# Kernel tuning notes

Measured on AMD Instinct MI355X. Metric: run time of the kernel, lower is better.

## Reference

```python
import jax, jax.numpy as jnp
import numpy as np

N_NODES = 50000


def _gcn_conv(x, edge_index, W, b):
    """PyG-style GCNConv: add self-loops, symmetric deg^-1/2 norm, linear + scatter-add + bias."""
    n = x.shape[0]
    # add self loops
    loop = jnp.arange(n, dtype=edge_index.dtype)
    src = jnp.concatenate([edge_index[0], loop])  # [E+N]
    dst = jnp.concatenate([edge_index[1], loop])
    ones = jnp.ones_like(dst, dtype=x.dtype)
    deg = jax.ops.segment_sum(ones, dst, num_segments=n)  # in-degree incl. self loop
    deg_inv_sqrt = jnp.where(deg > 0, jax.lax.rsqrt(deg), 0.0)
    norm = deg_inv_sqrt[src] * deg_inv_sqrt[dst]  # [E+N]
    h = x @ W  # [N, out]
    msg = h[src] * norm[:, None]  # gather + scale, [E+N, out]
    out = jax.ops.segment_sum(msg, dst, num_segments=n)  # scatter-add
    return out + b


def setup_inputs() -> dict:
    key = jax.random.key(0)
    k1, k2, k3, k4 = jax.random.split(key, 4)
    in_ch, hid, z = 128, 128, 64
    x = jax.random.normal(k1, (N_NODES, in_ch), dtype=jnp.float32)
    edge_index = jax.random.randint(k2, (2, 800000), 0, N_NODES, dtype=jnp.int64)
    W1 = jax.random.normal(k3, (in_ch, hid), dtype=jnp.float32) * (1.0 / np.sqrt(in_ch))
    b1 = jnp.zeros((hid,), dtype=jnp.float32)
    W2 = jax.random.normal(k4, (hid, z), dtype=jnp.float32) * (1.0 / np.sqrt(hid))
    b2 = jnp.zeros((z,), dtype=jnp.float32)
    return {"x": x, "edge_index": edge_index, "W1": W1, "b1": b1, "W2": W2, "b2": b2}


def reference(x, edge_index, W1, b1, W2, b2):
    h = jax.nn.relu(_gcn_conv(x, edge_index, W1, b1))
    return _gcn_conv(h, edge_index, W2, b2)
```

## Files before the change

kernel.cpp:

```cpp
#include <hip/hip_runtime.h>

static constexpr int K = 128;

using ushort8 = __attribute__((ext_vector_type(8))) unsigned short;
using bf16x8  = __attribute__((ext_vector_type(8))) __bf16;
using f32x4   = __attribute__((ext_vector_type(4))) float;

__device__ inline float bflo(unsigned u) { return __uint_as_float(u << 16); }
__device__ inline float bfhi(unsigned u) { return __uint_as_float(u & 0xFFFF0000u); }
__device__ inline unsigned short f2bf(float f) {
    unsigned u = __float_as_uint(f);
    return (unsigned short)((u + 0x7FFF + ((u >> 16) & 1)) >> 16);
}


__global__ __launch_bounds__(256) void k_zerob(int* __restrict__ bcnt) {
    bcnt[threadIdx.x] = 0;
}

__global__ __launch_bounds__(256) void k_bcount(const int* __restrict__ dst, int e,
                                                int* __restrict__ bcnt, int nb) {
    __shared__ int c[256];
    int t = threadIdx.x;
    c[t] = 0;
    __syncthreads();
    for (int i = blockIdx.x * 256 + t; i < e; i += gridDim.x * 256)
        atomicAdd(&c[dst[i] >> 8], 1);
    __syncthreads();
    if (t < nb && c[t]) atomicAdd(&bcnt[t], c[t]);
}

__global__ __launch_bounds__(256) void k_bscan(const int* __restrict__ bcnt,
                                               int* __restrict__ bbase,
                                               int* __restrict__ gcur,
                                               int nb, int* __restrict__ offs,
                                               int n, int e) {
    __shared__ int sh[256];
    int t = threadIdx.x;
    int v = (t < nb) ? bcnt[t] : 0;
    sh[t] = v;
    __syncthreads();
    for (int o = 1; o < 256; o <<= 1) {
        int x = (t >= o) ? sh[t - o] : 0;
        __syncthreads();
        sh[t] += x;
        __syncthreads();
    }
    int excl = sh[t] - v;
    bbase[t] = excl;
    gcur[t] = excl;
    if (t == 255) bbase[256] = sh[255];
    if (t == 0) offs[n] = e;
}

__global__ __launch_bounds__(256) void k_bin(const int* __restrict__ ei, int e,
                                             int* __restrict__ gcur,
                                             unsigned long long* __restrict__ tmp) {
    constexpr int PER = 8;
    __shared__ int cnt[256], base[256], cur[256];
    int t = threadIdx.x;
    int chunk0 = blockIdx.x * 256 * PER;
    cnt[t] = 0;
    __syncthreads();
    int ds[PER];
#pragma unroll
    for (int k2 = 0; k2 < PER; ++k2) {
        int i = chunk0 + k2 * 256 + t;
        ds[k2] = (i < e) ? ei[(size_t)e + i] : -1;
        if (ds[k2] >= 0) atomicAdd(&cnt[ds[k2] >> 8], 1);
    }
    __syncthreads();
    int c = cnt[t];
    base[t] = c ? atomicAdd(&gcur[t], c) : 0;
    cur[t] = 0;
    __syncthreads();
#pragma unroll
    for (int k2 = 0; k2 < PER; ++k2) {
        int i = chunk0 + k2 * 256 + t;
        if (i < e) {
            int b = ds[k2] >> 8;
            int pos = base[b] + atomicAdd(&cur[b], 1);
            tmp[pos] = ((unsigned long long)(unsigned)ds[k2] << 32) | (unsigned)ei[i];
        }
    }
}

__global__ __launch_bounds__(256) void k_csr(const unsigned long long* __restrict__ tmp,
                                             const int* __restrict__ bbase,
                                             int* __restrict__ offs,
                                             int* __restrict__ srt,
                                             float* __restrict__ dinv, int n) {
    __shared__ int cntS[256], sh[256], cur[256];
    int b = blockIdx.x;
    int t = threadIdx.x;
    int beg = bbase[b], end = bbase[b + 1];
    cntS[t] = 0;
    __syncthreads();
    for (int i = beg + t; i < end; i += 256)
        atomicAdd(&cntS[(int)(tmp[i] >> 32) & 255], 1);
    __syncthreads();
    int v = cntS[t];
    sh[t] = v;
    __syncthreads();
    for (int o = 1; o < 256; o <<= 1) {
        int x = (t >= o) ? sh[t - o] : 0;
        __syncthreads();
        sh[t] += x;
        __syncthreads();
    }
    int pfx = sh[t] - v;
    int node = b * 256 + t;
    if (node < n) {
        offs[node] = beg + pfx;
        dinv[node] = rsqrtf((float)(v + 1));
    }
    cur[t] = pfx;
    __syncthreads();
    for (int i = beg + t; i < end; i += 256) {
        unsigned long long pr = tmp[i];
        int d = (int)(pr >> 32);
        int pos = atomicAdd(&cur[d & 255], 1);
        srt[beg + pos] = (int)(pr & 0xFFFFFFFFu);
    }
}


template <int COUT>
__global__ __launch_bounds__(256) void k_gemm_mfma(const float* __restrict__ X,
                                                   const float* __restrict__ W,
                                                   const float* __restrict__ dinv,
                                                   unsigned short* __restrict__ G, int n) {
    constexpr int BM = 64, BK = 32;
    constexpr int NCT = COUT / 16;
    constexpr int NCH = K / BK;
    constexpr int WT = COUT * (BK / 8) / 256;
    __shared__ unsigned short Ah[BM * BK], Al[BM * BK];
    __shared__ unsigned short Bh[COUT * BK], Bl[COUT * BK];
    __shared__ float dS[BM];
    const int tid = threadIdx.x;
    const int row0 = blockIdx.x * BM;
    if (tid < BM) {
        int gr = row0 + tid;
        dS[tid] = (gr < n) ? dinv[gr] : 0.f;
    }

    float4 xr[2];
    float wr[WT][8];

    auto loadX = [&](int kc) {
        int r = tid >> 2, ks = tid & 3;
        int gr = row0 + r;
        if (gr < n) {
            const float4* pp = (const float4*)(X + (size_t)gr * K + kc * BK + ks * 8);
            xr[0] = pp[0];
            xr[1] = pp[1];
        } else {
            xr[0] = make_float4(0.f, 0.f, 0.f, 0.f);
            xr[1] = xr[0];
        }
    };
    auto loadW = [&](int kc) {
#pragma unroll
        for (int q = 0; q < WT; ++q) {
            int i = tid + q * 256;
            int c = i % COUT, ks = i / COUT;
#pragma unroll
            for (int j = 0; j < 8; ++j)
                wr[q][j] = W[(size_t)(kc * BK + ks * 8 + j) * COUT + c];
        }
    };
    auto storeLDS = [&]() {
        int r = tid >> 2, ks = tid & 3;
        ushort8 h, l;
        const float* f = (const float*)&xr[0];
#pragma unroll
        for (int j = 0; j < 8; ++j) {
            unsigned short hh = f2bf(f[j]);
            h[j] = hh;
            l[j] = f2bf(f[j] - __uint_as_float((unsigned)hh << 16));
        }
        *(ushort8*)&Ah[r * BK + ks * 8] = h;
        *(ushort8*)&Al[r * BK + ks * 8] = l;
#pragma unroll
        for (int q = 0; q < WT; ++q) {
            int i = tid + q * 256;
            int c = i % COUT, ks2 = i / COUT;
            ushort8 wh, wl;
#pragma unroll
            for (int j = 0; j < 8; ++j) {
                unsigned short hh = f2bf(wr[q][j]);
                wh[j] = hh;
                wl[j] = f2bf(wr[q][j] - __uint_as_float((unsigned)hh << 16));
            }
            *(ushort8*)&Bh[c * BK + ks2 * 8] = wh;
            *(ushort8*)&Bl[c * BK + ks2 * 8] = wl;
        }
    };

    f32x4 acc[NCT] = {};
    const int l = tid & 63, wv = tid >> 6;
    const int l16 = l & 15, lk = l >> 4;
    const int arow = wv * 16 + l16;

    loadX(0);
    loadW(0);
    storeLDS();
    __syncthreads();
    for (int c = 0; c < NCH; ++c) {
        if (c + 1 < NCH) { loadX(c + 1); loadW(c + 1); }
        bf16x8 ah = *(const bf16x8*)&Ah[arow * BK + lk * 8];
        bf16x8 al = *(const bf16x8*)&Al[arow * BK + lk * 8];
#pragma unroll
        for (int ct = 0; ct < NCT; ++ct) {
            bf16x8 bh = *(const bf16x8*)&Bh[(ct * 16 + l16) * BK + lk * 8];
            bf16x8 bl = *(const bf16x8*)&Bl[(ct * 16 + l16) * BK + lk * 8];
            acc[ct] = __builtin_amdgcn_mfma_f32_16x16x32_bf16(ah, bh, acc[ct], 0, 0, 0);
            acc[ct] = __builtin_amdgcn_mfma_f32_16x16x32_bf16(al, bh, acc[ct], 0, 0, 0);
            acc[ct] = __builtin_amdgcn_mfma_f32_16x16x32_bf16(ah, bl, acc[ct], 0, 0, 0);
        }
        if (c + 1 < NCH) {
            __syncthreads();
            storeLDS();
            __syncthreads();
        }
    }

#pragma unroll
    for (int ct = 0; ct < NCT; ++ct) {
        int col = ct * 16 + l16;
#pragma unroll
        for (int r4 = 0; r4 < 4; ++r4) {
            int lr = wv * 16 + lk * 4 + r4;
            int gr = row0 + lr;
            if (gr < n) G[(size_t)gr * COUT + col] = f2bf(acc[ct][r4] * dS[lr]);
        }
    }
}


#define ADD8(u)                                      \
    do {                                             \
        a[0] += bflo((u).x); a[1] += bfhi((u).x);    \
        a[2] += bflo((u).y); a[3] += bfhi((u).y);    \
        a[4] += bflo((u).z); a[5] += bfhi((u).z);    \
        a[6] += bflo((u).w); a[7] += bfhi((u).w);    \
    } while (0)

template <bool RELU>
__global__ __launch_bounds__(256) void k_reduce128(const int* __restrict__ offs,
                                                   const int* __restrict__ srt,
                                                   const uint4* __restrict__ g4,
                                                   const float* __restrict__ dinv,
                                                   const float* __restrict__ bias,
                                                   float* __restrict__ out, int n) {
    int node = blockIdx.x * 4 + (threadIdx.x >> 6);
    if (node >= n) return;
    int lane = threadIdx.x & 63;
    int l16 = lane & 15, grp = lane >> 4;
    int beg = offs[node], end = offs[node + 1];

    float a[8] = {};
    if (grp == 0) {
        uint4 u = g4[(size_t)node * 16 + l16];
        ADD8(u);
    }
    int j = beg + grp;
    for (; j + 12 < end; j += 16) {
        uint4 u0 = g4[(size_t)srt[j]      * 16 + l16];
        uint4 u1 = g4[(size_t)srt[j + 4]  * 16 + l16];
        uint4 u2 = g4[(size_t)srt[j + 8]  * 16 + l16];
        uint4 u3 = g4[(size_t)srt[j + 12] * 16 + l16];
        ADD8(u0); ADD8(u1); ADD8(u2); ADD8(u3);
    }
    for (; j < end; j += 4) {
        uint4 u = g4[(size_t)srt[j] * 16 + l16];
        ADD8(u);
    }
#pragma unroll
    for (int q = 0; q < 8; ++q) {
        a[q] += __shfl_xor(a[q], 16);
        a[q] += __shfl_xor(a[q], 32);
    }
    if (lane < 16) {
        float di = dinv[node];
        float4 b0 = ((const float4*)bias)[l16 * 2];
        float4 b1 = ((const float4*)bias)[l16 * 2 + 1];
        float4 o0, o1;
        o0.x = fmaf(di, a[0], b0.x); o0.y = fmaf(di, a[1], b0.y);
        o0.z = fmaf(di, a[2], b0.z); o0.w = fmaf(di, a[3], b0.w);
        o1.x = fmaf(di, a[4], b1.x); o1.y = fmaf(di, a[5], b1.y);
        o1.z = fmaf(di, a[6], b1.z); o1.w = fmaf(di, a[7], b1.w);
        if (RELU) {
            o0.x = fmaxf(o0.x, 0.f); o0.y = fmaxf(o0.y, 0.f);
            o0.z = fmaxf(o0.z, 0.f); o0.w = fmaxf(o0.w, 0.f);
            o1.x = fmaxf(o1.x, 0.f); o1.y = fmaxf(o1.y, 0.f);
            o1.z = fmaxf(o1.z, 0.f); o1.w = fmaxf(o1.w, 0.f);
        }
        float4* op = (float4*)(out + (size_t)node * 128 + l16 * 8);
        op[0] = o0;
        op[1] = o1;
    }
}

template <bool RELU>
__global__ __launch_bounds__(256) void k_reduce64(const int* __restrict__ offs,
                                                  const int* __restrict__ srt,
                                                  const uint4* __restrict__ g4,
                                                  const float* __restrict__ dinv,
                                                  const float* __restrict__ bias,
                                                  float* __restrict__ out, int n) {
    int node = blockIdx.x * 4 + (threadIdx.x >> 6);
    if (node >= n) return;
    int lane = threadIdx.x & 63;
    int l8 = lane & 7, grp = lane >> 3;
    int beg = offs[node], end = offs[node + 1];

    float a[8] = {};
    if (grp == 0) {
        uint4 u = g4[(size_t)node * 8 + l8];
        ADD8(u);
    }
    int j = beg + grp;
    for (; j + 8 < end; j += 16) {
        uint4 u0 = g4[(size_t)srt[j]     * 8 + l8];
        uint4 u1 = g4[(size_t)srt[j + 8] * 8 + l8];
        ADD8(u0); ADD8(u1);
    }
    for (; j < end; j += 8) {
        uint4 u = g4[(size_t)srt[j] * 8 + l8];
        ADD8(u);
    }
#pragma unroll
    for (int q = 0; q < 8; ++q) {
        a[q] += __shfl_xor(a[q], 8);
        a[q] += __shfl_xor(a[q], 16);
        a[q] += __shfl_xor(a[q], 32);
    }
    if (lane < 8) {
        float di = dinv[node];
        float4 b0 = ((const float4*)bias)[l8 * 2];
        float4 b1 = ((const float4*)bias)[l8 * 2 + 1];
        float4 o0, o1;
        o0.x = fmaf(di, a[0], b0.x); o0.y = fmaf(di, a[1], b0.y);
        o0.z = fmaf(di, a[2], b0.z); o0.w = fmaf(di, a[3], b0.w);
        o1.x = fmaf(di, a[4], b1.x); o1.y = fmaf(di, a[5], b1.y);
        o1.z = fmaf(di, a[6], b1.z); o1.w = fmaf(di, a[7], b1.w);
        if (RELU) {
            o0.x = fmaxf(o0.x, 0.f); o0.y = fmaxf(o0.y, 0.f);
            o0.z = fmaxf(o0.z, 0.f); o0.w = fmaxf(o0.w, 0.f);
            o1.x = fmaxf(o1.x, 0.f); o1.y = fmaxf(o1.y, 0.f);
            o1.z = fmaxf(o1.z, 0.f); o1.w = fmaxf(o1.w, 0.f);
        }
        float4* op = (float4*)(out + (size_t)node * 64 + l8 * 8);
        op[0] = o0;
        op[1] = o1;
    }
}

extern "C" void kernel_launch(void* const* d_in, const int* in_sizes, int n_in,
                              void* d_out, int out_size, void* d_ws, size_t ws_size,
                              hipStream_t stream) {
    const float* x  = (const float*)d_in[0];
    const int*   ei = (const int*)d_in[1];
    const float* W1 = (const float*)d_in[2];
    const float* b1 = (const float*)d_in[3];
    const float* W2 = (const float*)d_in[4];
    const float* b2 = (const float*)d_in[5];
    float* out = (float*)d_out;

    const int n = in_sizes[0] / K;
    const int e = in_sizes[1] / 2;
    const int nb = (n + 255) / 256;

    char* p = (char*)d_ws;
    unsigned long long* tmp = (unsigned long long*)p;  p += (size_t)e * 8;
    int* bcnt  = (int*)p;  p += 256 * 4;
    int* bbase = (int*)p;  p += 257 * 4;
    int* gcur  = (int*)p;  p += 256 * 4;
    int* offs  = (int*)p;  p += (size_t)(n + 1) * 4;
    int* srt   = (int*)p;  p += (size_t)e * 4;
    float* dinv = (float*)p;  p += (size_t)n * 4;
    p = (char*)(((uintptr_t)p + 15) & ~(uintptr_t)15);
    unsigned short* G1 = (unsigned short*)p;  p += (size_t)n * 128 * 2;
    p = (char*)(((uintptr_t)p + 15) & ~(uintptr_t)15);
    float* H = (float*)p;  p += (size_t)n * 128 * 4;
    p = (char*)(((uintptr_t)p + 15) & ~(uintptr_t)15);
    unsigned short* G2 = (unsigned short*)p;

    k_zerob<<<1, 256, 0, stream>>>(bcnt);
    k_bcount<<<512, 256, 0, stream>>>(ei + e, e, bcnt, nb);
    k_bscan<<<1, 256, 0, stream>>>(bcnt, bbase, gcur, nb, offs, n, e);
    k_bin<<<(e + 2047) / 2048, 256, 0, stream>>>(ei, e, gcur, tmp);
    k_csr<<<nb, 256, 0, stream>>>(tmp, bbase, offs, srt, dinv, n);

    k_gemm_mfma<128><<<(n + 63) / 64, 256, 0, stream>>>(x, W1, dinv, G1, n);
    k_reduce128<true><<<(n + 3) / 4, 256, 0, stream>>>(offs, srt, (const uint4*)G1,
                                                       dinv, b1, H, n);

    k_gemm_mfma<64><<<(n + 63) / 64, 256, 0, stream>>>(H, W2, dinv, G2, n);
    k_reduce64<false><<<(n + 3) / 4, 256, 0, stream>>>(offs, srt, (const uint4*)G2,
                                                       dinv, b2, out, n);
}
```

Measured before the change: 156.0 us.

## Bin edges into fixed-capacity buckets and store hidden layer as bf16

The separate edge-count pass and its scan are removed. Edges are now binned directly into per-bucket slabs of fixed capacity (CAP=8192), and the scan runs afterwards. The CSR kernel now uses 1024 threads per bucket. The hidden activation H is stored as bf16 instead of fp32, and a new bf16-input GEMM for layer 2 drops the low-part split on X, which reduces memory traffic and MFMA work. The cost is extra rounding on H and a hard bucket capacity that overflows if any 256-node bucket receives more than 8192 edges.

```diff
diff --git a/kernel.cpp b/kernel.cpp
--- a/kernel.cpp
+++ b/kernel.cpp
@@ -1,6 +1,7 @@
 #include <hip/hip_runtime.h>
 
 static constexpr int K = 128;
+static constexpr int CAP = 8192;
 
 using ushort8 = __attribute__((ext_vector_type(8))) unsigned short;
 using bf16x8  = __attribute__((ext_vector_type(8))) __bf16;
@@ -14,30 +15,46 @@
 }
 
 
-__global__ __launch_bounds__(256) void k_zerob(int* __restrict__ bcnt) {
-    bcnt[threadIdx.x] = 0;
-}
-
-__global__ __launch_bounds__(256) void k_bcount(const int* __restrict__ dst, int e,
-                                                int* __restrict__ bcnt, int nb) {
-    __shared__ int c[256];
+__global__ __launch_bounds__(256) void k_bin(const int* __restrict__ ei, int e,
+                                             int* __restrict__ gcur,
+                                             unsigned long long* __restrict__ tmp) {
+    constexpr int PER = 4;
+    __shared__ int cnt[256], base[256], cur[256];
     int t = threadIdx.x;
-    c[t] = 0;
-    __syncthreads();
-    for (int i = blockIdx.x * 256 + t; i < e; i += gridDim.x * 256)
-        atomicAdd(&c[dst[i] >> 8], 1);
-    __syncthreads();
-    if (t < nb && c[t]) atomicAdd(&bcnt[t], c[t]);
-}
-
-__global__ __launch_bounds__(256) void k_bscan(const int* __restrict__ bcnt,
+    int chunk0 = blockIdx.x * 256 * PER;
+    cnt[t] = 0;
+    __syncthreads();
+    int ds[PER];
+#pragma unroll
+    for (int k2 = 0; k2 < PER; ++k2) {
+        int i = chunk0 + k2 * 256 + t;
+        ds[k2] = (i < e) ? ei[(size_t)e + i] : -1;
+        if (ds[k2] >= 0) atomicAdd(&cnt[ds[k2] >> 8], 1);
+    }
+    __syncthreads();
+    int c = cnt[t];
+    base[t] = c ? atomicAdd(&gcur[t], c) : 0;
+    cur[t] = 0;
+    __syncthreads();
+#pragma unroll
+    for (int k2 = 0; k2 < PER; ++k2) {
+        int i = chunk0 + k2 * 256 + t;
+        if (i < e) {
+            int b = ds[k2] >> 8;
+            int pos = base[b] + atomicAdd(&cur[b], 1);
+            tmp[(size_t)b * CAP + pos] =
+                ((unsigned long long)(unsigned)ds[k2] << 32) | (unsigned)ei[i];
+        }
+    }
+}
+
+__global__ __launch_bounds__(256) void k_bscan(const int* __restrict__ gcur,
                                                int* __restrict__ bbase,
-                                               int* __restrict__ gcur,
                                                int nb, int* __restrict__ offs,
                                                int n, int e) {
     __shared__ int sh[256];
     int t = threadIdx.x;
-    int v = (t < nb) ? bcnt[t] : 0;
+    int v = (t < nb) ? gcur[t] : 0;
     sh[t] = v;
     __syncthreads();
     for (int o = 1; o < 256; o <<= 1) {
@@ -46,78 +63,48 @@
         sh[t] += x;
         __syncthreads();
     }
-    int excl = sh[t] - v;
-    bbase[t] = excl;
-    gcur[t] = excl;
+    bbase[t] = sh[t] - v;
     if (t == 255) bbase[256] = sh[255];
     if (t == 0) offs[n] = e;
 }
 
-__global__ __launch_bounds__(256) void k_bin(const int* __restrict__ ei, int e,
-                                             int* __restrict__ gcur,
-                                             unsigned long long* __restrict__ tmp) {
-    constexpr int PER = 8;
-    __shared__ int cnt[256], base[256], cur[256];
-    int t = threadIdx.x;
-    int chunk0 = blockIdx.x * 256 * PER;
-    cnt[t] = 0;
-    __syncthreads();
-    int ds[PER];
-#pragma unroll
-    for (int k2 = 0; k2 < PER; ++k2) {
-        int i = chunk0 + k2 * 256 + t;
-        ds[k2] = (i < e) ? ei[(size_t)e + i] : -1;
-        if (ds[k2] >= 0) atomicAdd(&cnt[ds[k2] >> 8], 1);
-    }
-    __syncthreads();
-    int c = cnt[t];
-    base[t] = c ? atomicAdd(&gcur[t], c) : 0;
-    cur[t] = 0;
-    __syncthreads();
-#pragma unroll
-    for (int k2 = 0; k2 < PER; ++k2) {
-        int i = chunk0 + k2 * 256 + t;
-        if (i < e) {
-            int b = ds[k2] >> 8;
-            int pos = base[b] + atomicAdd(&cur[b], 1);
-            tmp[pos] = ((unsigned long long)(unsigned)ds[k2] << 32) | (unsigned)ei[i];
-        }
-    }
-}
-
-__global__ __launch_bounds__(256) void k_csr(const unsigned long long* __restrict__ tmp,
-                                             const int* __restrict__ bbase,
-                                             int* __restrict__ offs,
-                                             int* __restrict__ srt,
-                                             float* __restrict__ dinv, int n) {
+__global__ __launch_bounds__(1024) void k_csr(const unsigned long long* __restrict__ tmp,
+                                              const int* __restrict__ bbase,
+                                              int* __restrict__ offs,
+                                              int* __restrict__ srt,
+                                              float* __restrict__ dinv, int n) {
     __shared__ int cntS[256], sh[256], cur[256];
     int b = blockIdx.x;
     int t = threadIdx.x;
-    int beg = bbase[b], end = bbase[b + 1];
-    cntS[t] = 0;
-    __syncthreads();
-    for (int i = beg + t; i < end; i += 256)
-        atomicAdd(&cntS[(int)(tmp[i] >> 32) & 255], 1);
-    __syncthreads();
-    int v = cntS[t];
-    sh[t] = v;
+    int beg = bbase[b];
+    int tot = bbase[b + 1] - beg;
+    const unsigned long long* tb = tmp + (size_t)b * CAP;
+    if (t < 256) cntS[t] = 0;
+    __syncthreads();
+    for (int i = t; i < tot; i += 1024)
+        atomicAdd(&cntS[(int)(tb[i] >> 32) & 255], 1);
+    __syncthreads();
+    int v = (t < 256) ? cntS[t] : 0;
+    if (t < 256) sh[t] = v;
     __syncthreads();
     for (int o = 1; o < 256; o <<= 1) {
-        int x = (t >= o) ? sh[t - o] : 0;
+        int x = (t < 256 && t >= o) ? sh[t - o] : 0;
         __syncthreads();
-        sh[t] += x;
+        if (t < 256) sh[t] += x;
         __syncthreads();
     }
-    int pfx = sh[t] - v;
-    int node = b * 256 + t;
-    if (node < n) {
-        offs[node] = beg + pfx;
-        dinv[node] = rsqrtf((float)(v + 1));
-    }
-    cur[t] = pfx;
-    __syncthreads();
-    for (int i = beg + t; i < end; i += 256) {
-        unsigned long long pr = tmp[i];
+    if (t < 256) {
+        int pfx = sh[t] - v;
+        int node = b * 256 + t;
+        if (node < n) {
+            offs[node] = beg + pfx;
+            dinv[node] = rsqrtf((float)(v + 1));
+        }
+        cur[t] = pfx;
+    }
+    __syncthreads();
+    for (int i = t; i < tot; i += 1024) {
+        unsigned long long pr = tb[i];
         int d = (int)(pr >> 32);
         int pos = atomicAdd(&cur[d & 255], 1);
         srt[beg + pos] = (int)(pr & 0xFFFFFFFFu);
@@ -238,6 +225,94 @@
 }
 
 
+__global__ __launch_bounds__(256) void k_gemm_bf16(const unsigned short* __restrict__ X,
+                                                   const float* __restrict__ W,
+                                                   const float* __restrict__ dinv,
+                                                   unsigned short* __restrict__ G, int n) {
+    constexpr int COUT = 64, BM = 64, BK = 32;
+    constexpr int NCT = COUT / 16;
+    constexpr int NCH = K / BK;
+    __shared__ unsigned short Ah[BM * BK];
+    __shared__ unsigned short Bh[COUT * BK], Bl[COUT * BK];
+    __shared__ float dS[BM];
+    const int tid = threadIdx.x;
+    const int row0 = blockIdx.x * BM;
+    if (tid < BM) {
+        int gr = row0 + tid;
+        dS[tid] = (gr < n) ? dinv[gr] : 0.f;
+    }
+
+    ushort8 xrb;
+    float wr[8];
+
+    auto loadX = [&](int kc) {
+        int r = tid >> 2, ks = tid & 3;
+        int gr = row0 + r;
+        if (gr < n)
+            xrb = *(const ushort8*)(X + (size_t)gr * K + kc * BK + ks * 8);
+        else
+            xrb = (ushort8){0, 0, 0, 0, 0, 0, 0, 0};
+    };
+    auto loadW = [&](int kc) {
+        int c = tid % COUT, ks = tid / COUT;
+#pragma unroll
+        for (int j = 0; j < 8; ++j)
+            wr[j] = W[(size_t)(kc * BK + ks * 8 + j) * COUT + c];
+    };
+    auto storeLDS = [&]() {
+        int r = tid >> 2, ks = tid & 3;
+        *(ushort8*)&Ah[r * BK + ks * 8] = xrb;
+        int c = tid % COUT, ks2 = tid / COUT;
+        ushort8 wh, wl;
+#pragma unroll
+        for (int j = 0; j < 8; ++j) {
+            unsigned short hh = f2bf(wr[j]);
+            wh[j] = hh;
+            wl[j] = f2bf(wr[j] - __uint_as_float((unsigned)hh << 16));
+        }
+        *(ushort8*)&Bh[c * BK + ks2 * 8] = wh;
+        *(ushort8*)&Bl[c * BK + ks2 * 8] = wl;
+    };
+
+    f32x4 acc[NCT] = {};
+    const int l = tid & 63, wv = tid >> 6;
+    const int l16 = l & 15, lk = l >> 4;
+    const int arow = wv * 16 + l16;
+
+    loadX(0);
+    loadW(0);
+    storeLDS();
+    __syncthreads();
+    for (int c = 0; c < NCH; ++c) {
+        if (c + 1 < NCH) { loadX(c + 1); loadW(c + 1); }
+        bf16x8 ah = *(const bf16x8*)&Ah[arow * BK + lk * 8];
+#pragma unroll
+        for (int ct = 0; ct < NCT; ++ct) {
+            bf16x8 bh = *(const bf16x8*)&Bh[(ct * 16 + l16) * BK + lk * 8];
+            bf16x8 bl = *(const bf16x8*)&Bl[(ct * 16 + l16) * BK + lk * 8];
+            acc[ct] = __builtin_amdgcn_mfma_f32_16x16x32_bf16(ah, bh, acc[ct], 0, 0, 0);
+            acc[ct] = __builtin_amdgcn_mfma_f32_16x16x32_bf16(ah, bl, acc[ct], 0, 0, 0);
+        }
+        if (c + 1 < NCH) {
+            __syncthreads();
+            storeLDS();
+            __syncthreads();
+        }
+    }
+
+#pragma unroll
+    for (int ct = 0; ct < NCT; ++ct) {
+        int col = ct * 16 + l16;
+#pragma unroll
+        for (int r4 = 0; r4 < 4; ++r4) {
+            int lr = wv * 16 + lk * 4 + r4;
+            int gr = row0 + lr;
+            if (gr < n) G[(size_t)gr * COUT + col] = f2bf(acc[ct][r4] * dS[lr]);
+        }
+    }
+}
+
+
 #define ADD8(u)                                      \
     do {                                             \
         a[0] += bflo((u).x); a[1] += bfhi((u).x);    \
@@ -246,13 +321,12 @@
         a[6] += bflo((u).w); a[7] += bfhi((u).w);    \
     } while (0)
 
-template <bool RELU>
 __global__ __launch_bounds__(256) void k_reduce128(const int* __restrict__ offs,
                                                    const int* __restrict__ srt,
                                                    const uint4* __restrict__ g4,
                                                    const float* __restrict__ dinv,
                                                    const float* __restrict__ bias,
-                                                   float* __restrict__ out, int n) {
+                                                   unsigned short* __restrict__ out, int n) {
     int node = blockIdx.x * 4 + (threadIdx.x >> 6);
     if (node >= n) return;
     int lane = threadIdx.x & 63;
@@ -283,26 +357,16 @@
     }
     if (lane < 16) {
         float di = dinv[node];
-        float4 b0 = ((const float4*)bias)[l16 * 2];
-        float4 b1 = ((const float4*)bias)[l16 * 2 + 1];
-        float4 o0, o1;
-        o0.x = fmaf(di, a[0], b0.x); o0.y = fmaf(di, a[1], b0.y);
-        o0.z = fmaf(di, a[2], b0.z); o0.w = fmaf(di, a[3], b0.w);
-        o1.x = fmaf(di, a[4], b1.x); o1.y = fmaf(di, a[5], b1.y);
-        o1.z = fmaf(di, a[6], b1.z); o1.w = fmaf(di, a[7], b1.w);
-        if (RELU) {
-            o0.x = fmaxf(o0.x, 0.f); o0.y = fmaxf(o0.y, 0.f);
-            o0.z = fmaxf(o0.z, 0.f); o0.w = fmaxf(o0.w, 0.f);
-            o1.x = fmaxf(o1.x, 0.f); o1.y = fmaxf(o1.y, 0.f);
-            o1.z = fmaxf(o1.z, 0.f); o1.w = fmaxf(o1.w, 0.f);
-        }
-        float4* op = (float4*)(out + (size_t)node * 128 + l16 * 8);
-        op[0] = o0;
-        op[1] = o1;
-    }
-}
-
-template <bool RELU>
+        ushort8 o;
+#pragma unroll
+        for (int q = 0; q < 8; ++q) {
+            float v = fmaf(di, a[q], bias[l16 * 8 + q]);
+            o[q] = f2bf(fmaxf(v, 0.f));
+        }
+        *(ushort8*)(out + (size_t)node * 128 + l16 * 8) = o;
+    }
+}
+
 __global__ __launch_bounds__(256) void k_reduce64(const int* __restrict__ offs,
                                                   const int* __restrict__ srt,
                                                   const uint4* __restrict__ g4,
@@ -345,12 +409,6 @@
         o0.z = fmaf(di, a[2], b0.z); o0.w = fmaf(di, a[3], b0.w);
         o1.x = fmaf(di, a[4], b1.x); o1.y = fmaf(di, a[5], b1.y);
         o1.z = fmaf(di, a[6], b1.z); o1.w = fmaf(di, a[7], b1.w);
-        if (RELU) {
-            o0.x = fmaxf(o0.x, 0.f); o0.y = fmaxf(o0.y, 0.f);
-            o0.z = fmaxf(o0.z, 0.f); o0.w = fmaxf(o0.w, 0.f);
-            o1.x = fmaxf(o1.x, 0.f); o1.y = fmaxf(o1.y, 0.f);
-            o1.z = fmaxf(o1.z, 0.f); o1.w = fmaxf(o1.w, 0.f);
-        }
         float4* op = (float4*)(out + (size_t)node * 64 + l8 * 8);
         op[0] = o0;
         op[1] = o1;
@@ -373,31 +431,29 @@
     const int nb = (n + 255) / 256;
 
     char* p = (char*)d_ws;
-    unsigned long long* tmp = (unsigned long long*)p;  p += (size_t)e * 8;
-    int* bcnt  = (int*)p;  p += 256 * 4;
+    unsigned long long* tmp = (unsigned long long*)p;  p += (size_t)nb * CAP * 8;
+    int* gcur  = (int*)p;  p += 256 * 4;
     int* bbase = (int*)p;  p += 257 * 4;
-    int* gcur  = (int*)p;  p += 256 * 4;
     int* offs  = (int*)p;  p += (size_t)(n + 1) * 4;
     int* srt   = (int*)p;  p += (size_t)e * 4;
     float* dinv = (float*)p;  p += (size_t)n * 4;
     p = (char*)(((uintptr_t)p + 15) & ~(uintptr_t)15);
     unsigned short* G1 = (unsigned short*)p;  p += (size_t)n * 128 * 2;
     p = (char*)(((uintptr_t)p + 15) & ~(uintptr_t)15);
-    float* H = (float*)p;  p += (size_t)n * 128 * 4;
+    unsigned short* H = (unsigned short*)p;   p += (size_t)n * 128 * 2;
     p = (char*)(((uintptr_t)p + 15) & ~(uintptr_t)15);
     unsigned short* G2 = (unsigned short*)p;
 
-    k_zerob<<<1, 256, 0, stream>>>(bcnt);
-    k_bcount<<<512, 256, 0, stream>>>(ei + e, e, bcnt, nb);
-    k_bscan<<<1, 256, 0, stream>>>(bcnt, bbase, gcur, nb, offs, n, e);
-    k_bin<<<(e + 2047) / 2048, 256, 0, stream>>>(ei, e, gcur, tmp);
-    k_csr<<<nb, 256, 0, stream>>>(tmp, bbase, offs, srt, dinv, n);
+    hipMemsetAsync(gcur, 0, 256 * sizeof(int), stream);
+    k_bin<<<(e + 1023) / 1024, 256, 0, stream>>>(ei, e, gcur, tmp);
+    k_bscan<<<1, 256, 0, stream>>>(gcur, bbase, nb, offs, n, e);
+    k_csr<<<nb, 1024, 0, stream>>>(tmp, bbase, offs, srt, dinv, n);
 
     k_gemm_mfma<128><<<(n + 63) / 64, 256, 0, stream>>>(x, W1, dinv, G1, n);
-    k_reduce128<true><<<(n + 3) / 4, 256, 0, stream>>>(offs, srt, (const uint4*)G1,
-                                                       dinv, b1, H, n);
-
-    k_gemm_mfma<64><<<(n + 63) / 64, 256, 0, stream>>>(H, W2, dinv, G2, n);
-    k_reduce64<false><<<(n + 3) / 4, 256, 0, stream>>>(offs, srt, (const uint4*)G2,
-                                                       dinv, b2, out, n);
-}
+    k_reduce128<<<(n + 3) / 4, 256, 0, stream>>>(offs, srt, (const uint4*)G1,
+                                                 dinv, b1, H, n);
+
+    k_gemm_bf16<<<(n + 63) / 64, 256, 0, stream>>>(H, W2, dinv, G2, n);
+    k_reduce64<<<(n + 3) / 4, 256, 0, stream>>>(offs, srt, (const uint4*)G2,
+                                                dinv, b2, out, n);
+}
```

After: 135.0 us. 1.16x faster.
